# Kernel optimization log

Measured on AMD Instinct MI355X. Metric: run time of the kernel, lower is better.

The kernel has to match this reference:

```python
import jax, jax.numpy as jnp
import numpy as np

D_MODEL = 1024
N_HEADS = 16
D_HEAD = D_MODEL // N_HEADS
QLEN = 512
MLEN = 512
BATCH = 8


def setup_inputs() -> dict:
    key = jax.random.key(0)
    ks = jax.random.split(key, 12)
    s = 0.02
    inputs = jax.random.normal(ks[0], (QLEN, BATCH, D_MODEL), jnp.float32)
    r = jax.random.normal(ks[1], (QLEN + MLEN, 1, D_MODEL), jnp.float32)
    u = jax.random.normal(ks[2], (N_HEADS, D_HEAD), jnp.float32) * s
    v = jax.random.normal(ks[3], (N_HEADS, D_HEAD), jnp.float32) * s
    mem = jax.random.normal(ks[4], (MLEN, BATCH, D_MODEL), jnp.float32)
    # attention params (Transformer-XL style): fused qkv, r-projection, output proj
    W_qkv = jax.random.normal(ks[5], (D_MODEL, 3 * D_MODEL), jnp.float32) * s
    W_r = jax.random.normal(ks[6], (D_MODEL, D_MODEL), jnp.float32) * s
    W_o = jax.random.normal(ks[7], (D_MODEL, D_MODEL), jnp.float32) * s
    # GRU params: input-hidden and hidden-hidden for gates (r, z, n), torch layout
    W_ih = jax.random.normal(ks[8], (3 * D_MODEL, D_MODEL), jnp.float32) * s
    W_hh = jax.random.normal(ks[9], (3 * D_MODEL, D_MODEL), jnp.float32) * s
    b_ih = jax.random.normal(ks[10], (3 * D_MODEL,), jnp.float32) * s
    b_hh = jax.random.normal(ks[11], (3 * D_MODEL,), jnp.float32) * s
    h0 = jnp.zeros((BATCH, D_MODEL), jnp.float32)
    return dict(inputs=inputs, r=r, u=u, v=v, mem=mem, W_qkv=W_qkv, W_r=W_r,
                W_o=W_o, W_ih=W_ih, W_hh=W_hh, b_ih=b_ih, b_hh=b_hh, h0=h0)


def _rel_shift(x):
    # x: [q, k, b, h] -> Transformer-XL relative shift
    q, k, b, h = x.shape
    zero_pad = jnp.zeros((q, 1, b, h), x.dtype)
    x_padded = jnp.concatenate([zero_pad, x], axis=1)        # [q, k+1, b, h]
    x_padded = x_padded.reshape(k + 1, q, b, h)
    return x_padded[1:].reshape(q, k, b, h)


def _attention(inputs, r, u, v, mem, W_qkv, W_r, W_o):
    qlen, bsz, _ = inputs.shape
    cat = jnp.concatenate([mem, inputs], axis=0)             # [klen, b, d]
    klen = cat.shape[0]
    qkv = cat @ W_qkv                                        # [klen, b, 3d]
    w_head_q, w_head_k, w_head_v = jnp.split(qkv, 3, axis=-1)
    w_head_q = w_head_q[-qlen:]                              # [q, b, d]
    r_head_k = (r[:, 0, :] @ W_r).reshape(klen, N_HEADS, D_HEAD)  # [k, h, dh]

    q_ = w_head_q.reshape(qlen, bsz, N_HEADS, D_HEAD)
    k_ = w_head_k.reshape(klen, bsz, N_HEADS, D_HEAD)
    v_ = w_head_v.reshape(klen, bsz, N_HEADS, D_HEAD)

    AC = jnp.einsum('ibhd,jbhd->ijbh', q_ + u[None, None], k_)
    BD = jnp.einsum('ibhd,jhd->ijbh', q_ + v[None, None], r_head_k)
    BD = _rel_shift(BD)
    scale = 1.0 / np.sqrt(D_HEAD)
    attn_score = (AC + BD) * scale                           # [q, k, b, h]

    # causal mask with memory: query i attends to keys j <= i + mlen
    mlen = klen - qlen
    i = jnp.arange(qlen)[:, None]
    j = jnp.arange(klen)[None, :]
    mask = j > (i + mlen)                                    # [q, k]
    attn_score = jnp.where(mask[:, :, None, None], -jnp.inf, attn_score)

    attn_prob = jax.nn.softmax(attn_score, axis=1)
    attn_vec = jnp.einsum('ijbh,jbhd->ibhd', attn_prob, v_)
    attn_vec = attn_vec.reshape(qlen, bsz, D_MODEL)
    return attn_vec @ W_o                                    # [q, b, d]


def _gru(x, h0, W_ih, W_hh, b_ih, b_hh):
    # x: [T, B, D]; torch GRU cell math
    Wi_r, Wi_z, Wi_n = jnp.split(W_ih, 3, axis=0)
    Wh_r, Wh_z, Wh_n = jnp.split(W_hh, 3, axis=0)
    bi_r, bi_z, bi_n = jnp.split(b_ih, 3)
    bh_r, bh_z, bh_n = jnp.split(b_hh, 3)

    # precompute input projections for all timesteps
    xr = x @ Wi_r.T + bi_r
    xz = x @ Wi_z.T + bi_z
    xn = x @ Wi_n.T + bi_n

    def step(h, xs):
        xr_t, xz_t, xn_t = xs
        r = jax.nn.sigmoid(xr_t + h @ Wh_r.T + bh_r)
        z = jax.nn.sigmoid(xz_t + h @ Wh_z.T + bh_z)
        n = jnp.tanh(xn_t + r * (h @ Wh_n.T + bh_n))
        h_new = (1.0 - z) * n + z * h
        return h_new, h_new

    _, ys = jax.lax.scan(step, h0, (xr, xz, xn))
    return ys                                                # [T, B, D]


def reference(inputs, r, u, v, mem, W_qkv, W_r, W_o, W_ih, W_hh, b_ih, b_hh, h0):
    y = _attention(inputs, r, u, v, mem, W_qkv, W_r, W_o)
    return _gru(y, h0, W_ih, W_hh, b_ih, b_hh)
```

## Files before the change

### kernel.cpp

```cpp
#include <hip/hip_runtime.h>
#include <math.h>


typedef short bf16x8 __attribute__((ext_vector_type(8)));
typedef float f32x4 __attribute__((ext_vector_type(4)));

union FragU { uint4 u; bf16x8 h; };

__device__ inline void split2(float x0, float x1, unsigned& hi, unsigned& lo) {
    unsigned u0 = __float_as_uint(x0), u1 = __float_as_uint(x1);
    float h0 = __uint_as_float(u0 & 0xffff0000u);
    float h1 = __uint_as_float(u1 & 0xffff0000u);
    unsigned l0 = __float_as_uint(x0 - h0), l1 = __float_as_uint(x1 - h1);
    hi = (u0 >> 16) | (u1 & 0xffff0000u);
    lo = (l0 >> 16) | (l1 & 0xffff0000u);
}

__device__ __forceinline__ unsigned long long ld_coh64(const void* p) {
    return __hip_atomic_load((const unsigned long long*)p, __ATOMIC_RELAXED,
                             __HIP_MEMORY_SCOPE_AGENT);
}
__device__ __forceinline__ void st_coh64(void* p, unsigned long long v) {
    __hip_atomic_store((unsigned long long*)p, v, __ATOMIC_RELAXED,
                       __HIP_MEMORY_SCOPE_AGENT);
}

template<bool TR>
__global__ __launch_bounds__(256) void prep_w(
    const float* __restrict__ W, unsigned* __restrict__ out, int Nr, int K, int ldw)
{
    int idx = blockIdx.x * 256 + threadIdx.x;
    int cpr = K >> 3;
    if (idx >= Nr * cpr) return;
    int n, c;
    if (TR) { n = idx % Nr; c = idx / Nr; }
    else    { c = idx % cpr; n = idx / cpr; }
    int kt = c >> 2, j = c & 3;
    int k = kt * 32 + j * 8;
    float x[8];
    #pragma unroll
    for (int i = 0; i < 8; ++i)
        x[i] = TR ? W[(size_t)(k + i) * ldw + n] : W[(size_t)n * ldw + k + i];
    unsigned h[4], l[4];
    split2(x[0], x[1], h[0], l[0]);
    split2(x[2], x[3], h[1], l[1]);
    split2(x[4], x[5], h[2], l[2]);
    split2(x[6], x[7], h[3], l[3]);
    unsigned* base = out + (size_t)n * K + kt * 32;
    *(uint4*)(base + (((2 * j) ^ (n & 7)) * 4))     = make_uint4(h[0], h[1], h[2], h[3]);
    *(uint4*)(base + (((2 * j + 1) ^ (n & 7)) * 4)) = make_uint4(l[0], l[1], l[2], l[3]);
}

template<int AMODE, bool BIAS>
__global__ __launch_bounds__(256) void gemm_mfma(
    const float* __restrict__ A, const float* __restrict__ A2,
    const unsigned* __restrict__ Bp, const float* __restrict__ bias,
    float* __restrict__ C, int M, int N, int K, int lda, int ldc)
{
    __shared__ uint4 Ab[1024];
    __shared__ uint4 Bb[1024];
    int tid = threadIdx.x;
    int lane = tid & 63, wid = tid >> 6;
    int wr = wid >> 1, wc = wid & 1;
    int n0 = blockIdx.x * 128, m0 = blockIdx.y * 128;
    int r15 = lane & 15, s = lane >> 4;

    f32x4 acc[4][4];
    #pragma unroll
    for (int i = 0; i < 4; ++i)
        #pragma unroll
        for (int j = 0; j < 4; ++j) acc[i][j] = 0.0f;

    for (int kt = 0; kt < (K >> 5); ++kt) {
        int k0 = kt * 32;
        #pragma unroll
        for (int q = 0; q < 2; ++q) {
            int idx = q * 256 + tid;
            int row = idx >> 2, j = idx & 3;
            const float* ap;
            if (AMODE == 1) {
                int gm = m0 + row;
                ap = (gm < 4096) ? (A + (size_t)gm * lda) : (A2 + (size_t)(gm - 4096) * lda);
            } else {
                ap = A + (size_t)(m0 + row) * lda;
            }
            float4 x0 = *(const float4*)(ap + k0 + j * 8);
            float4 x1 = *(const float4*)(ap + k0 + j * 8 + 4);
            unsigned h[4], l[4];
            split2(x0.x, x0.y, h[0], l[0]);
            split2(x0.z, x0.w, h[1], l[1]);
            split2(x1.x, x1.y, h[2], l[2]);
            split2(x1.z, x1.w, h[3], l[3]);
            Ab[row * 8 + (((2 * j) ^ (row & 7)))]     = make_uint4(h[0], h[1], h[2], h[3]);
            Ab[row * 8 + (((2 * j + 1) ^ (row & 7)))] = make_uint4(l[0], l[1], l[2], l[3]);
        }
        #pragma unroll
        for (int q = 0; q < 4; ++q) {
            int idx = q * 256 + tid;
            int row = idx >> 3, slot = idx & 7;
            Bb[idx] = *(const uint4*)(Bp + (size_t)(n0 + row) * K + k0 + slot * 4);
        }
        __syncthreads();
        FragU ahi[4], alo[4], bhi[4], blo[4];
        #pragma unroll
        for (int f = 0; f < 4; ++f) {
            int ar = wr * 64 + f * 16 + r15;
            ahi[f].u = Ab[ar * 8 + ((2 * s) ^ (ar & 7))];
            alo[f].u = Ab[ar * 8 + ((2 * s + 1) ^ (ar & 7))];
            int br = wc * 64 + f * 16 + r15;
            bhi[f].u = Bb[br * 8 + ((2 * s) ^ (br & 7))];
            blo[f].u = Bb[br * 8 + ((2 * s + 1) ^ (br & 7))];
        }
        #pragma unroll
        for (int fi = 0; fi < 4; ++fi)
            #pragma unroll
            for (int fj = 0; fj < 4; ++fj) {
                acc[fi][fj] = __builtin_amdgcn_mfma_f32_16x16x32_bf16(ahi[fi].h, bhi[fj].h, acc[fi][fj], 0, 0, 0);
                acc[fi][fj] = __builtin_amdgcn_mfma_f32_16x16x32_bf16(ahi[fi].h, blo[fj].h, acc[fi][fj], 0, 0, 0);
                acc[fi][fj] = __builtin_amdgcn_mfma_f32_16x16x32_bf16(alo[fi].h, bhi[fj].h, acc[fi][fj], 0, 0, 0);
            }
        __syncthreads();
    }
    int r4 = (lane >> 4) * 4;
    #pragma unroll
    for (int fj = 0; fj < 4; ++fj) {
        int n = n0 + wc * 64 + fj * 16 + r15;
        float bv = BIAS ? bias[n] : 0.f;
        #pragma unroll
        for (int fi = 0; fi < 4; ++fi) {
            int m = m0 + wr * 64 + fi * 16 + r4;
            #pragma unroll
            for (int r = 0; r < 4; ++r)
                C[(size_t)(m + r) * ldc + n] = acc[fi][fj][r] + bv;
        }
    }
}

__global__ __launch_bounds__(256) void attn_fused(
    const float* __restrict__ qkv, const float* __restrict__ rk,
    const float* __restrict__ u_, const float* __restrict__ v_,
    float* __restrict__ y1)
{
    __shared__ float qu[64][68], qv[64][68], Kt[64][68], Vt[64][68];
    __shared__ float RKs[128][68];
    __shared__ float S[64][68];
    __shared__ float mrow[64], lrow[64], scalef[64];
    __shared__ float pmax[64][16], psum[64][16];

    int tid = threadIdx.x;
    int it = blockIdx.x, b = blockIdx.y, h = blockIdx.z;
    int i0 = it * 64;
    int ti = tid >> 4, tj = tid & 15;

    {
        int r = tid >> 2, c0 = (tid & 3) * 16;
        size_t base = ((size_t)(i0 + r + 512) * 8 + b) * 3072 + h * 64;
        #pragma unroll
        for (int q = 0; q < 4; ++q) {
            int c = c0 + q * 4;
            float4 qq = *(const float4*)&qkv[base + c];
            float4 uu = *(const float4*)&u_[h * 64 + c];
            float4 vv = *(const float4*)&v_[h * 64 + c];
            *(float4*)&qu[r][c] = make_float4(qq.x + uu.x, qq.y + uu.y, qq.z + uu.z, qq.w + uu.w);
            *(float4*)&qv[r][c] = make_float4(qq.x + vv.x, qq.y + vv.y, qq.z + vv.z, qq.w + vv.w);
        }
    }
    if (tid < 64) { mrow[tid] = -1e30f; lrow[tid] = 0.f; }

    float Od[4][4] = {};
    int njt = it + 9;

    for (int jt = 0; jt < njt; ++jt) {
        int j0 = jt * 64;
        __syncthreads();
        {
            int r = tid >> 2, c0 = (tid & 3) * 16;
            size_t kb = ((size_t)(j0 + r) * 8 + b) * 3072 + 1024 + h * 64;
            #pragma unroll
            for (int q = 0; q < 4; ++q) {
                int c = c0 + q * 4;
                *(float4*)&Kt[r][c] = *(const float4*)&qkv[kb + c];
                *(float4*)&Vt[r][c] = *(const float4*)&qkv[kb + 1024 + c];
            }
        }
        {
            int r2 = tid >> 1, c0 = (tid & 1) * 32;
            int jj = j0 - i0 + 448 + r2;
            jj = jj < 0 ? 0 : (jj > 1023 ? 1023 : jj);
            size_t rb = (size_t)jj * 1024 + h * 64;
            #pragma unroll
            for (int q = 0; q < 8; ++q) {
                int c = c0 + q * 4;
                *(float4*)&RKs[r2][c] = *(const float4*)&rk[rb + c];
            }
        }
        __syncthreads();

        float acc[4][4] = {};
        int jlb = (tj - ti) * 4 + 60;
        #pragma unroll 4
        for (int d4 = 0; d4 < 64; d4 += 4) {
            float4 Aq[4], Cq[4], Kv[4], Rv[7];
            #pragma unroll
            for (int i = 0; i < 4; ++i) {
                Aq[i] = *(float4*)&qu[ti * 4 + i][d4];
                Cq[i] = *(float4*)&qv[ti * 4 + i][d4];
                Kv[i] = *(float4*)&Kt[tj * 4 + i][d4];
            }
            #pragma unroll
            for (int t = 0; t < 7; ++t)
                Rv[t] = *(float4*)&RKs[jlb + t][d4];
            #pragma unroll
            for (int i = 0; i < 4; ++i)
                #pragma unroll
                for (int j = 0; j < 4; ++j) {
                    float4 kk = Kv[j];
                    float4 rr = Rv[j - i + 3];
                    acc[i][j] += Aq[i].x * kk.x + Aq[i].y * kk.y + Aq[i].z * kk.z + Aq[i].w * kk.w
                               + Cq[i].x * rr.x + Cq[i].y * rr.y + Cq[i].z * rr.z + Cq[i].w * rr.w;
                }
        }
        #pragma unroll
        for (int i = 0; i < 4; ++i) {
            int gi = i0 + ti * 4 + i;
            float mx = -1e30f;
            #pragma unroll
            for (int j = 0; j < 4; ++j) {
                int gj = j0 + tj * 4 + j;
                float vS = acc[i][j] * 0.125f;
                if (gj > gi + 512) vS = -1e30f;
                acc[i][j] = vS;
                mx = fmaxf(mx, vS);
            }
            pmax[ti * 4 + i][tj] = mx;
        }
        __syncthreads();
        if (tid < 64) {
            float mo = mrow[tid], mn = mo;
            #pragma unroll
            for (int t = 0; t < 16; ++t) mn = fmaxf(mn, pmax[tid][t]);
            mrow[tid] = mn;
            scalef[tid] = __expf(mo - mn);
        }
        __syncthreads();
        #pragma unroll
        for (int i = 0; i < 4; ++i) {
            int ri = ti * 4 + i;
            float mn = mrow[ri];
            float4 pv;
            pv.x = __expf(acc[i][0] - mn);
            pv.y = __expf(acc[i][1] - mn);
            pv.z = __expf(acc[i][2] - mn);
            pv.w = __expf(acc[i][3] - mn);
            *(float4*)&S[ri][tj * 4] = pv;
            psum[ri][tj] = pv.x + pv.y + pv.z + pv.w;
            float scl = scalef[ri];
            #pragma unroll
            for (int j2 = 0; j2 < 4; ++j2) Od[i][j2] *= scl;
        }
        __syncthreads();
        if (tid < 64) {
            float s = 0.f;
            #pragma unroll
            for (int t = 0; t < 16; ++t) s += psum[tid][t];
            lrow[tid] = lrow[tid] * scalef[tid] + s;
        }
        #pragma unroll 4
        for (int jb = 0; jb < 64; jb += 4) {
            float4 p0 = *(float4*)&S[ti * 4 + 0][jb];
            float4 p1 = *(float4*)&S[ti * 4 + 1][jb];
            float4 p2 = *(float4*)&S[ti * 4 + 2][jb];
            float4 p3 = *(float4*)&S[ti * 4 + 3][jb];
            float4 v0 = *(float4*)&Vt[jb + 0][tj * 4];
            float4 v1 = *(float4*)&Vt[jb + 1][tj * 4];
            float4 v2 = *(float4*)&Vt[jb + 2][tj * 4];
            float4 v3 = *(float4*)&Vt[jb + 3][tj * 4];
            float4 pr[4] = {p0, p1, p2, p3};
            #pragma unroll
            for (int i = 0; i < 4; ++i) {
                Od[i][0] += pr[i].x * v0.x + pr[i].y * v1.x + pr[i].z * v2.x + pr[i].w * v3.x;
                Od[i][1] += pr[i].x * v0.y + pr[i].y * v1.y + pr[i].z * v2.y + pr[i].w * v3.y;
                Od[i][2] += pr[i].x * v0.z + pr[i].y * v1.z + pr[i].z * v2.z + pr[i].w * v3.z;
                Od[i][3] += pr[i].x * v0.w + pr[i].y * v1.w + pr[i].z * v2.w + pr[i].w * v3.w;
            }
        }
    }
    __syncthreads();
    #pragma unroll
    for (int i = 0; i < 4; ++i) {
        int ri = ti * 4 + i;
        float inv = 1.f / lrow[ri];
        float4 o = make_float4(Od[i][0] * inv, Od[i][1] * inv, Od[i][2] * inv, Od[i][3] * inv);
        *(float4*)&y1[((size_t)(i0 + ri) * 8 + b) * 1024 + h * 64 + tj * 4] = o;
    }
}

__global__ __launch_bounds__(256) void prep_whh(
    const float* __restrict__ Whh, uint4* __restrict__ outp)
{
    int idx = blockIdx.x * 256 + threadIdx.x;
    if (idx >= 393216) return;
    int lane = idx & 63;
    int rest = idx >> 6;
    int gate = rest % 3;
    int kt   = (rest / 3) & 31;
    int g64  = rest / 96;
    int n = gate * 1024 + g64 * 16 + (lane & 15);
    int k = kt * 32 + (lane >> 4) * 8;
    const float* src = Whh + (size_t)n * 1024 + k;
    float4 x0 = *(const float4*)src, x1 = *(const float4*)(src + 4);
    unsigned h[4], l[4];
    split2(x0.x, x0.y, h[0], l[0]);
    split2(x0.z, x0.w, h[1], l[1]);
    split2(x1.x, x1.y, h[2], l[2]);
    split2(x1.z, x1.w, h[3], l[3]);
    outp[((size_t)rest * 2 + 0) * 64 + lane] = make_uint4(h[0], h[1], h[2], h[3]);
    outp[((size_t)rest * 2 + 1) * 64 + lane] = make_uint4(l[0], l[1], l[2], l[3]);
}

__global__ __launch_bounds__(256, 1) void gru_persist3(
    const float* __restrict__ h0, float* __restrict__ hA, float* __restrict__ hB,
    const uint4* __restrict__ WhhG, const float* __restrict__ bhh,
    const float* __restrict__ xg, float* __restrict__ out,
    unsigned* __restrict__ flags)
{
    __shared__ uint4 Bf[4096];
    __shared__ float red[3][64][4];
    int tid = threadIdx.x;
    int lane = tid & 63, wv = tid >> 6;
    int g64 = blockIdx.x;

    int col = lane & 15;
    int d0 = g64 * 16 + (lane >> 4) * 4;
    bool act = (wv == 0) && (col < 8);
    float4 br4 = make_float4(0, 0, 0, 0), bz4 = br4, bn4 = br4, hprev4 = br4;
    if (act) {
        br4 = *(const float4*)&bhh[d0];
        bz4 = *(const float4*)&bhh[1024 + d0];
        bn4 = *(const float4*)&bhh[2048 + d0];
        hprev4 = *(const float4*)&h0[col * 1024 + d0];
    }
    const uint4* wb = WhhG + (size_t)g64 * 12288 + (wv < 3 ? wv : 0) * 128 + lane;

    int toff[4], tkt[4], tln[4];
    const unsigned* tfl[4];
    #pragma unroll
    for (int i = 0; i < 4; ++i) {
        int s = i * 256 + tid;
        int b = s & 7, oct = (s >> 3) & 3, kt = s >> 5;
        toff[i] = b * 1024 + kt * 32 + oct * 8;
        tkt[i] = kt;
        tln[i] = oct * 16 + b;
        tfl[i] = &flags[(size_t)(2 * kt + (oct >> 1)) * 16];
    }

    for (int t = 0; t < 512; ++t) {
        const float* hi_ = (t == 0) ? h0 : ((t & 1) ? hA : hB);
        float* ho = (t & 1) ? hB : hA;

        float4 xr4, xz4, xn4;
        if (act) {
            size_t xb = ((size_t)t * 8 + col) * 3072 + d0;
            xr4 = *(const float4*)&xg[xb];
            xz4 = *(const float4*)&xg[xb + 1024];
            xn4 = *(const float4*)&xg[xb + 2048];
        }

        uint4 wA[16], wB[16];
        if (wv < 3) {
            #pragma unroll
            for (int q = 0; q < 8; ++q) {
                wA[2 * q]     = wb[q * 384];
                wA[2 * q + 1] = wb[q * 384 + 64];
            }
        }

        unsigned long long hq[16];
        unsigned tgt = (unsigned)t;
        #pragma unroll
        for (int i = 0; i < 4; ++i) {
            if (t > 0) {
                while (__hip_atomic_load(tfl[i], __ATOMIC_RELAXED,
                                         __HIP_MEMORY_SCOPE_AGENT) < tgt) {}
            }
            const float* hp = hi_ + toff[i];
            #pragma unroll
            for (int q = 0; q < 4; ++q) hq[i * 4 + q] = ld_coh64(hp + q * 2);
        }
        #pragma unroll
        for (int i = 0; i < 4; ++i) {
            float x[8];
            #pragma unroll
            for (int q = 0; q < 4; ++q) {
                x[2 * q]     = __uint_as_float((unsigned)(hq[i * 4 + q] & 0xffffffffu));
                x[2 * q + 1] = __uint_as_float((unsigned)(hq[i * 4 + q] >> 32));
            }
            unsigned hh[4], ll[4];
            split2(x[0], x[1], hh[0], ll[0]);
            split2(x[2], x[3], hh[1], ll[1]);
            split2(x[4], x[5], hh[2], ll[2]);
            split2(x[6], x[7], hh[3], ll[3]);
            Bf[(tkt[i] * 2 + 0) * 64 + tln[i]] = make_uint4(hh[0], hh[1], hh[2], hh[3]);
            Bf[(tkt[i] * 2 + 1) * 64 + tln[i]] = make_uint4(ll[0], ll[1], ll[2], ll[3]);
        }
        __syncthreads();

        #define GRU_LOAD(dst, c0)                                   \
            _Pragma("unroll")                                       \
            for (int q = 0; q < 8; ++q) {                           \
                dst[2 * q]     = wb[((c0) * 8 + q) * 384];          \
                dst[2 * q + 1] = wb[((c0) * 8 + q) * 384 + 64];     \
            }
        #define GRU_COMP(src, c0, a)                                \
            _Pragma("unroll")                                       \
            for (int q = 0; q < 8; ++q) {                           \
                int kt = (c0) * 8 + q;                              \
                FragU ah, al, bh, bl;                               \
                ah.u = src[2 * q]; al.u = src[2 * q + 1];           \
                bh.u = Bf[(kt * 2 + 0) * 64 + lane];                \
                bl.u = Bf[(kt * 2 + 1) * 64 + lane];                \
                a = __builtin_amdgcn_mfma_f32_16x16x32_bf16(ah.h, bh.h, a, 0, 0, 0); \
                a = __builtin_amdgcn_mfma_f32_16x16x32_bf16(ah.h, bl.h, a, 0, 0, 0); \
                a = __builtin_amdgcn_mfma_f32_16x16x32_bf16(al.h, bh.h, a, 0, 0, 0); \
            }
        if (wv < 3) {
            f32x4 a0 = 0.0f, a1 = 0.0f, a2 = 0.0f, a3 = 0.0f;
            GRU_LOAD(wB, 1);
            GRU_COMP(wA, 0, a0);
            GRU_LOAD(wA, 2);
            GRU_COMP(wB, 1, a1);
            GRU_LOAD(wB, 3);
            GRU_COMP(wA, 2, a2);
            GRU_COMP(wB, 3, a3);
            f32x4 av = (a0 + a1) + (a2 + a3);
            *(f32x4*)&red[wv][lane][0] = av;
        }
        #undef GRU_LOAD
        #undef GRU_COMP
        __syncthreads();

        float hn[4];
        if (act) {
            f32x4 aR = *(f32x4*)&red[0][lane][0];
            f32x4 aZ = *(f32x4*)&red[1][lane][0];
            f32x4 aN = *(f32x4*)&red[2][lane][0];
            float xr[4] = {xr4.x, xr4.y, xr4.z, xr4.w};
            float xz[4] = {xz4.x, xz4.y, xz4.z, xz4.w};
            float xn[4] = {xn4.x, xn4.y, xn4.z, xn4.w};
            float hp[4] = {hprev4.x, hprev4.y, hprev4.z, hprev4.w};
            float br[4] = {br4.x, br4.y, br4.z, br4.w};
            float bz[4] = {bz4.x, bz4.y, bz4.z, bz4.w};
            float bn[4] = {bn4.x, bn4.y, bn4.z, bn4.w};
            #pragma unroll
            for (int r = 0; r < 4; ++r) {
                float rr = 1.f / (1.f + __expf(-(xr[r] + aR[r] + br[r])));
                float zz = 1.f / (1.f + __expf(-(xz[r] + aZ[r] + bz[r])));
                float nn = tanhf(xn[r] + rr * (aN[r] + bn[r]));
                hn[r] = (1.f - zz) * nn + zz * hp[r];
            }
            unsigned long long v01 = (unsigned long long)__float_as_uint(hn[0])
                                   | ((unsigned long long)__float_as_uint(hn[1]) << 32);
            unsigned long long v23 = (unsigned long long)__float_as_uint(hn[2])
                                   | ((unsigned long long)__float_as_uint(hn[3]) << 32);
            st_coh64(ho + col * 1024 + d0, v01);
            st_coh64(ho + col * 1024 + d0 + 2, v23);
        }
        if (wv == 0) {
            asm volatile("s_waitcnt vmcnt(0)" ::: "memory");
            __builtin_amdgcn_sched_barrier(0);
            if (tid == 0 && t != 511)
                __hip_atomic_store(&flags[(size_t)g64 * 16], (unsigned)(t + 1),
                                   __ATOMIC_RELAXED, __HIP_MEMORY_SCOPE_AGENT);
        }
        if (act) {
            *(float4*)&out[((size_t)t * 8 + col) * 1024 + d0] =
                make_float4(hn[0], hn[1], hn[2], hn[3]);
            hprev4 = make_float4(hn[0], hn[1], hn[2], hn[3]);
        }
    }
}

__global__ __launch_bounds__(192, 1) void gru_step_mfma(
    const float* __restrict__ hin, float* __restrict__ hout,
    const uint4* __restrict__ WhhG, const float* __restrict__ bhh,
    const float* __restrict__ xg, float* __restrict__ out, int t)
{
    __shared__ uint4 Bf[4096];
    __shared__ float red[3][64][4];
    int tid = threadIdx.x;
    int lane = tid & 63, wv = tid >> 6;
    int g64 = blockIdx.x;

    int col = lane & 15;
    int d0 = g64 * 16 + (lane >> 4) * 4;
    bool act = (wv == 0) && (col < 8);
    float4 xr4, xz4, xn4, hp4, br4, bz4, bn4;
    if (act) {
        size_t xb = ((size_t)t * 8 + col) * 3072 + d0;
        xr4 = *(const float4*)&xg[xb];
        xz4 = *(const float4*)&xg[xb + 1024];
        xn4 = *(const float4*)&xg[xb + 2048];
        hp4 = *(const float4*)&hin[col * 1024 + d0];
        br4 = *(const float4*)&bhh[d0];
        bz4 = *(const float4*)&bhh[1024 + d0];
        bn4 = *(const float4*)&bhh[2048 + d0];
    }

    const uint4* wb = WhhG + (size_t)g64 * 12288 + wv * 128 + lane;
    uint4 wA[16], wB[16];
    #pragma unroll
    for (int q = 0; q < 8; ++q) {
        wA[2 * q]     = wb[q * 384];
        wA[2 * q + 1] = wb[q * 384 + 64];
    }

    for (int s = tid; s < 1024; s += 192) {
        int b = s & 7, oct = (s >> 3) & 3, kt = s >> 5;
        const float* hp = hin + b * 1024 + kt * 32 + oct * 8;
        float4 x0 = *(const float4*)hp, x1 = *(const float4*)(hp + 4);
        unsigned hh[4], ll[4];
        split2(x0.x, x0.y, hh[0], ll[0]);
        split2(x0.z, x0.w, hh[1], ll[1]);
        split2(x1.x, x1.y, hh[2], ll[2]);
        split2(x1.z, x1.w, hh[3], ll[3]);
        int ln = oct * 16 + b;
        Bf[(kt * 2 + 0) * 64 + ln] = make_uint4(hh[0], hh[1], hh[2], hh[3]);
        Bf[(kt * 2 + 1) * 64 + ln] = make_uint4(ll[0], ll[1], ll[2], ll[3]);
    }
    __syncthreads();

    f32x4 acc = 0.0f;
    #define GRU_LOAD(dst, c0)                                   \
        _Pragma("unroll")                                       \
        for (int q = 0; q < 8; ++q) {                           \
            dst[2 * q]     = wb[((c0) * 8 + q) * 384];          \
            dst[2 * q + 1] = wb[((c0) * 8 + q) * 384 + 64];     \
        }
    #define GRU_COMP(src, c0)                                   \
        _Pragma("unroll")                                       \
        for (int q = 0; q < 8; ++q) {                           \
            int kt = (c0) * 8 + q;                              \
            FragU ah, al, bh, bl;                               \
            ah.u = src[2 * q]; al.u = src[2 * q + 1];           \
            bh.u = Bf[(kt * 2 + 0) * 64 + lane];                \
            bl.u = Bf[(kt * 2 + 1) * 64 + lane];                \
            acc = __builtin_amdgcn_mfma_f32_16x16x32_bf16(ah.h, bh.h, acc, 0, 0, 0); \
            acc = __builtin_amdgcn_mfma_f32_16x16x32_bf16(ah.h, bl.h, acc, 0, 0, 0); \
            acc = __builtin_amdgcn_mfma_f32_16x16x32_bf16(al.h, bh.h, acc, 0, 0, 0); \
        }
    GRU_LOAD(wB, 1);
    GRU_COMP(wA, 0);
    GRU_LOAD(wA, 2);
    GRU_COMP(wB, 1);
    GRU_LOAD(wB, 3);
    GRU_COMP(wA, 2);
    GRU_COMP(wB, 3);
    #undef GRU_LOAD
    #undef GRU_COMP

    *(f32x4*)&red[wv][lane][0] = acc;
    __syncthreads();

    if (act) {
        f32x4 aR = *(f32x4*)&red[0][lane][0];
        f32x4 aZ = *(f32x4*)&red[1][lane][0];
        f32x4 aN = *(f32x4*)&red[2][lane][0];
        float xr[4] = {xr4.x, xr4.y, xr4.z, xr4.w};
        float xz[4] = {xz4.x, xz4.y, xz4.z, xz4.w};
        float xn[4] = {xn4.x, xn4.y, xn4.z, xn4.w};
        float hp[4] = {hp4.x, hp4.y, hp4.z, hp4.w};
        float br[4] = {br4.x, br4.y, br4.z, br4.w};
        float bz[4] = {bz4.x, bz4.y, bz4.z, bz4.w};
        float bn[4] = {bn4.x, bn4.y, bn4.z, bn4.w};
        float hn[4];
        #pragma unroll
        for (int r = 0; r < 4; ++r) {
            float rr = 1.f / (1.f + __expf(-(xr[r] + aR[r] + br[r])));
            float zz = 1.f / (1.f + __expf(-(xz[r] + aZ[r] + bz[r])));
            float nn = tanhf(xn[r] + rr * (aN[r] + bn[r]));
            hn[r] = (1.f - zz) * nn + zz * hp[r];
        }
        float4 hv = make_float4(hn[0], hn[1], hn[2], hn[3]);
        *(float4*)&hout[col * 1024 + d0] = hv;
        *(float4*)&out[((size_t)t * 8 + col) * 1024 + d0] = hv;
    }
}

extern "C" void kernel_launch(void* const* d_in, const int* in_sizes, int n_in,
                              void* d_out, int out_size, void* d_ws, size_t ws_size,
                              hipStream_t stream) {
    (void)in_sizes; (void)n_in; (void)out_size; (void)ws_size;
    const float* inputs = (const float*)d_in[0];
    const float* r_in   = (const float*)d_in[1];
    const float* u_in   = (const float*)d_in[2];
    const float* v_in   = (const float*)d_in[3];
    const float* mem    = (const float*)d_in[4];
    const float* Wqkv   = (const float*)d_in[5];
    const float* Wr     = (const float*)d_in[6];
    const float* Wo     = (const float*)d_in[7];
    const float* Wih    = (const float*)d_in[8];
    const float* Whh    = (const float*)d_in[9];
    const float* bih    = (const float*)d_in[10];
    const float* bhh    = (const float*)d_in[11];
    const float* h0     = (const float*)d_in[12];
    float* out = (float*)d_out;
    float* ws = (float*)d_ws;

    float*    qkv   = ws;
    float*    rk    = ws + 25165824;
    float*    y1    = ws + 26214400;
    float*    y2    = ws + 30408704;
    float*    xg    = ws + 34603008;
    float*    hA    = ws + 47185920;
    float*    hB    = ws + 47194112;
    unsigned* WqkvP = (unsigned*)(ws + 47202304);
    unsigned* WrP   = (unsigned*)(ws + 50348032);
    unsigned* WoP   = (unsigned*)(ws + 51396608);
    unsigned* WihP  = (unsigned*)(ws + 52445184);
    unsigned* flags = (unsigned*)(ws + 55590912);
    uint4*    WhhG  = (uint4*)qkv;

    dim3 blk(256);
    prep_w<true ><<<1536, blk, 0, stream>>>(Wqkv, WqkvP, 3072, 1024, 3072);
    prep_w<true ><<< 512, blk, 0, stream>>>(Wr,   WrP,   1024, 1024, 1024);
    prep_w<true ><<< 512, blk, 0, stream>>>(Wo,   WoP,   1024, 1024, 1024);
    prep_w<false><<<1536, blk, 0, stream>>>(Wih,  WihP,  3072, 1024, 1024);
    hipMemsetAsync(flags, 0, 4096, stream);

    gemm_mfma<1, false><<<dim3(24, 64), blk, 0, stream>>>(
        mem, inputs, WqkvP, nullptr, qkv, 8192, 3072, 1024, 1024, 3072);
    gemm_mfma<0, false><<<dim3(8, 8), blk, 0, stream>>>(
        r_in, nullptr, WrP, nullptr, rk, 1024, 1024, 1024, 1024, 1024);
    attn_fused<<<dim3(8, 8, 16), blk, 0, stream>>>(qkv, rk, u_in, v_in, y1);
    prep_whh<<<1536, blk, 0, stream>>>(Whh, WhhG);
    gemm_mfma<0, false><<<dim3(8, 32), blk, 0, stream>>>(
        y1, nullptr, WoP, nullptr, y2, 4096, 1024, 1024, 1024, 1024);
    gemm_mfma<0, true><<<dim3(24, 32), blk, 0, stream>>>(
        y2, nullptr, WihP, bih, xg, 4096, 3072, 1024, 1024, 3072);

    {
        const float* a0 = h0; float* a1 = hA; float* a2 = hB;
        const uint4* a3 = WhhG; const float* a4 = bhh; const float* a5 = xg;
        float* a6 = out; unsigned* a7 = flags;
        void* args[8] = {&a0, &a1, &a2, &a3, &a4, &a5, &a6, &a7};
        hipError_t e = hipLaunchCooperativeKernel((void*)gru_persist3,
                                                  dim3(64), dim3(256), args, 0, stream);
        if (e != hipSuccess) {
            const float* hin = h0;
            for (int s = 0; s < 512; ++s) {
                float* hp = (s & 1) ? hB : hA;
                gru_step_mfma<<<64, dim3(192), 0, stream>>>(hin, hp, WhhG, bhh, xg, out, s);
                hin = hp;
            }
        }
    }
}
```

Baseline: 4.827 ms.

## Replace per-block step flags with tag-stamped hidden-state words in GRU kernel

The persistent GRU kernel no longer publishes a per-block flag after a vmcnt wait. Each hidden-state value is now stored as a 64-bit word that holds the step number in the high half and the float bits in the low half, in double buffers. Consumers spin on the data itself until every word carries the expected tag. This removes the store-then-flag round trip and the extra barrier on the sequential critical path. In exchange it doubles the hidden-state traffic, and every polling retry reloads the full 16-word chunk.

```diff
diff --git a/kernel.cpp b/kernel.cpp
--- a/kernel.cpp
+++ b/kernel.cpp
@@ -318,11 +318,11 @@
     outp[((size_t)rest * 2 + 1) * 64 + lane] = make_uint4(l[0], l[1], l[2], l[3]);
 }
 
-__global__ __launch_bounds__(256, 1) void gru_persist3(
-    const float* __restrict__ h0, float* __restrict__ hA, float* __restrict__ hB,
+__global__ __launch_bounds__(256, 1) void gru_persist4(
+    const float* __restrict__ h0,
+    unsigned long long* __restrict__ tb0, unsigned long long* __restrict__ tb1,
     const uint4* __restrict__ WhhG, const float* __restrict__ bhh,
-    const float* __restrict__ xg, float* __restrict__ out,
-    unsigned* __restrict__ flags)
+    const float* __restrict__ xg, float* __restrict__ out)
 {
     __shared__ uint4 Bf[4096];
     __shared__ float red[3][64][4];
@@ -343,7 +343,6 @@
     const uint4* wb = WhhG + (size_t)g64 * 12288 + (wv < 3 ? wv : 0) * 128 + lane;
 
     int toff[4], tkt[4], tln[4];
-    const unsigned* tfl[4];
     #pragma unroll
     for (int i = 0; i < 4; ++i) {
         int s = i * 256 + tid;
@@ -351,13 +350,9 @@
         toff[i] = b * 1024 + kt * 32 + oct * 8;
         tkt[i] = kt;
         tln[i] = oct * 16 + b;
-        tfl[i] = &flags[(size_t)(2 * kt + (oct >> 1)) * 16];
     }
 
     for (int t = 0; t < 512; ++t) {
-        const float* hi_ = (t == 0) ? h0 : ((t & 1) ? hA : hB);
-        float* ho = (t & 1) ? hB : hA;
-
         float4 xr4, xz4, xn4;
         if (act) {
             size_t xb = ((size_t)t * 8 + col) * 3072 + d0;
@@ -365,7 +360,6 @@
             xz4 = *(const float4*)&xg[xb + 1024];
             xn4 = *(const float4*)&xg[xb + 2048];
         }
-
         uint4 wA[16], wB[16];
         if (wv < 3) {
             #pragma unroll
@@ -375,33 +369,51 @@
             }
         }
 
-        unsigned long long hq[16];
-        unsigned tgt = (unsigned)t;
-        #pragma unroll
-        for (int i = 0; i < 4; ++i) {
-            if (t > 0) {
-                while (__hip_atomic_load(tfl[i], __ATOMIC_RELAXED,
-                                         __HIP_MEMORY_SCOPE_AGENT) < tgt) {}
-            }
-            const float* hp = hi_ + toff[i];
-            #pragma unroll
-            for (int q = 0; q < 4; ++q) hq[i * 4 + q] = ld_coh64(hp + q * 2);
-        }
-        #pragma unroll
-        for (int i = 0; i < 4; ++i) {
-            float x[8];
-            #pragma unroll
-            for (int q = 0; q < 4; ++q) {
-                x[2 * q]     = __uint_as_float((unsigned)(hq[i * 4 + q] & 0xffffffffu));
-                x[2 * q + 1] = __uint_as_float((unsigned)(hq[i * 4 + q] >> 32));
-            }
-            unsigned hh[4], ll[4];
-            split2(x[0], x[1], hh[0], ll[0]);
-            split2(x[2], x[3], hh[1], ll[1]);
-            split2(x[4], x[5], hh[2], ll[2]);
-            split2(x[6], x[7], hh[3], ll[3]);
-            Bf[(tkt[i] * 2 + 0) * 64 + tln[i]] = make_uint4(hh[0], hh[1], hh[2], hh[3]);
-            Bf[(tkt[i] * 2 + 1) * 64 + tln[i]] = make_uint4(ll[0], ll[1], ll[2], ll[3]);
+        if (t == 0) {
+            #pragma unroll
+            for (int i = 0; i < 4; ++i) {
+                const float* hp = h0 + toff[i];
+                float4 x0 = *(const float4*)hp, x1 = *(const float4*)(hp + 4);
+                unsigned hh[4], ll[4];
+                split2(x0.x, x0.y, hh[0], ll[0]);
+                split2(x0.z, x0.w, hh[1], ll[1]);
+                split2(x1.x, x1.y, hh[2], ll[2]);
+                split2(x1.z, x1.w, hh[3], ll[3]);
+                Bf[(tkt[i] * 2 + 0) * 64 + tln[i]] = make_uint4(hh[0], hh[1], hh[2], hh[3]);
+                Bf[(tkt[i] * 2 + 1) * 64 + tln[i]] = make_uint4(ll[0], ll[1], ll[2], ll[3]);
+            }
+        } else {
+            const unsigned long long* tb = (t & 1) ? tb1 : tb0;
+            unsigned tg = (unsigned)t;
+            #pragma unroll
+            for (int g = 0; g < 2; ++g) {
+                unsigned long long v[16];
+                for (;;) {
+                    #pragma unroll
+                    for (int j = 0; j < 16; ++j)
+                        v[j] = ld_coh64(tb + toff[g * 2 + (j >> 3)] + (j & 7));
+                    bool ok = true;
+                    #pragma unroll
+                    for (int j = 0; j < 16; ++j)
+                        ok = ok && ((unsigned)(v[j] >> 32) == tg);
+                    if (ok) break;
+                }
+                #pragma unroll
+                for (int i2 = 0; i2 < 2; ++i2) {
+                    int i = g * 2 + i2;
+                    float x[8];
+                    #pragma unroll
+                    for (int q = 0; q < 8; ++q)
+                        x[q] = __uint_as_float((unsigned)(v[i2 * 8 + q] & 0xffffffffu));
+                    unsigned hh[4], ll[4];
+                    split2(x[0], x[1], hh[0], ll[0]);
+                    split2(x[2], x[3], hh[1], ll[1]);
+                    split2(x[4], x[5], hh[2], ll[2]);
+                    split2(x[6], x[7], hh[3], ll[3]);
+                    Bf[(tkt[i] * 2 + 0) * 64 + tln[i]] = make_uint4(hh[0], hh[1], hh[2], hh[3]);
+                    Bf[(tkt[i] * 2 + 1) * 64 + tln[i]] = make_uint4(ll[0], ll[1], ll[2], ll[3]);
+                }
+            }
         }
         __syncthreads();
 
@@ -439,7 +451,6 @@
         #undef GRU_COMP
         __syncthreads();
 
-        float hn[4];
         if (act) {
             f32x4 aR = *(f32x4*)&red[0][lane][0];
             f32x4 aZ = *(f32x4*)&red[1][lane][0];
@@ -451,6 +462,7 @@
             float br[4] = {br4.x, br4.y, br4.z, br4.w};
             float bz[4] = {bz4.x, bz4.y, bz4.z, bz4.w};
             float bn[4] = {bn4.x, bn4.y, bn4.z, bn4.w};
+            float hn[4];
             #pragma unroll
             for (int r = 0; r < 4; ++r) {
                 float rr = 1.f / (1.f + __expf(-(xr[r] + aR[r] + br[r])));
@@ -458,21 +470,13 @@
                 float nn = tanhf(xn[r] + rr * (aN[r] + bn[r]));
                 hn[r] = (1.f - zz) * nn + zz * hp[r];
             }
-            unsigned long long v01 = (unsigned long long)__float_as_uint(hn[0])
-                                   | ((unsigned long long)__float_as_uint(hn[1]) << 32);
-            unsigned long long v23 = (unsigned long long)__float_as_uint(hn[2])
-                                   | ((unsigned long long)__float_as_uint(hn[3]) << 32);
-            st_coh64(ho + col * 1024 + d0, v01);
-            st_coh64(ho + col * 1024 + d0 + 2, v23);
-        }
-        if (wv == 0) {
-            asm volatile("s_waitcnt vmcnt(0)" ::: "memory");
-            __builtin_amdgcn_sched_barrier(0);
-            if (tid == 0 && t != 511)
-                __hip_atomic_store(&flags[(size_t)g64 * 16], (unsigned)(t + 1),
-                                   __ATOMIC_RELAXED, __HIP_MEMORY_SCOPE_AGENT);
-        }
-        if (act) {
+            unsigned long long* tbn = ((t + 1) & 1) ? tb1 : tb0;
+            unsigned long long tagw = ((unsigned long long)(unsigned)(t + 1)) << 32;
+            int base = col * 1024 + d0;
+            st_coh64(tbn + base + 0, tagw | (unsigned long long)__float_as_uint(hn[0]));
+            st_coh64(tbn + base + 1, tagw | (unsigned long long)__float_as_uint(hn[1]));
+            st_coh64(tbn + base + 2, tagw | (unsigned long long)__float_as_uint(hn[2]));
+            st_coh64(tbn + base + 3, tagw | (unsigned long long)__float_as_uint(hn[3]));
             *(float4*)&out[((size_t)t * 8 + col) * 1024 + d0] =
                 make_float4(hn[0], hn[1], hn[2], hn[3]);
             hprev4 = make_float4(hn[0], hn[1], hn[2], hn[3]);
@@ -617,7 +621,8 @@
     unsigned* WrP   = (unsigned*)(ws + 50348032);
     unsigned* WoP   = (unsigned*)(ws + 51396608);
     unsigned* WihP  = (unsigned*)(ws + 52445184);
-    unsigned* flags = (unsigned*)(ws + 55590912);
+    unsigned long long* tb0 = (unsigned long long*)(ws + 55590912);
+    unsigned long long* tb1 = (unsigned long long*)(ws + 55607296);
     uint4*    WhhG  = (uint4*)qkv;
 
     dim3 blk(256);
@@ -625,7 +630,7 @@
     prep_w<true ><<< 512, blk, 0, stream>>>(Wr,   WrP,   1024, 1024, 1024);
     prep_w<true ><<< 512, blk, 0, stream>>>(Wo,   WoP,   1024, 1024, 1024);
     prep_w<false><<<1536, blk, 0, stream>>>(Wih,  WihP,  3072, 1024, 1024);
-    hipMemsetAsync(flags, 0, 4096, stream);
+    hipMemsetAsync(tb0, 0, 131072, stream);
 
     gemm_mfma<1, false><<<dim3(24, 64), blk, 0, stream>>>(
         mem, inputs, WqkvP, nullptr, qkv, 8192, 3072, 1024, 1024, 3072);
@@ -639,11 +644,12 @@
         y2, nullptr, WihP, bih, xg, 4096, 3072, 1024, 1024, 3072);
 
     {
-        const float* a0 = h0; float* a1 = hA; float* a2 = hB;
+        const float* a0 = h0;
+        unsigned long long* a1 = tb0; unsigned long long* a2 = tb1;
         const uint4* a3 = WhhG; const float* a4 = bhh; const float* a5 = xg;
-        float* a6 = out; unsigned* a7 = flags;
-        void* args[8] = {&a0, &a1, &a2, &a3, &a4, &a5, &a6, &a7};
-        hipError_t e = hipLaunchCooperativeKernel((void*)gru_persist3,
+        float* a6 = out;
+        void* args[7] = {&a0, &a1, &a2, &a3, &a4, &a5, &a6};
+        hipError_t e = hipLaunchCooperativeKernel((void*)gru_persist4,
                                                   dim3(64), dim3(256), args, 0, stream);
         if (e != hipSuccess) {
             const float* hin = h0;
```

Measured after the change: 6.798 ms. 40.8% more time.
